# Kernel tuning notes

Hardware: AMD Instinct MI355X
Metric: run time of the kernel (lower is better)

## Reference

```python
import jax, jax.numpy as jnp
import numpy as np

EPS = 1e-5  # BatchNorm2d eps; BN in eval mode with running_mean=0, running_var=1

def conv_bn_relu(x, W, g, b):
    # x: [B, Cin, N, K]; W: [Cout, Cin] (1x1 conv). BN eval: (y-0)/sqrt(1+eps)*g + b, then ReLU.
    y = jnp.einsum('oc,bcnk->bonk', W, x)
    scale = (g / jnp.sqrt(1.0 + EPS))[None, :, None, None]
    return jax.nn.relu(y * scale + b[None, :, None, None])

def gather_neighbour(pc, idx):
    # pc: [B, N, d]; idx: [B, N, K] -> [B, N, K, d]
    B, N, K = idx.shape
    flat = idx.reshape(B, N * K, 1)
    return jnp.take_along_axis(pc, flat, axis=1).reshape(B, N, K, pc.shape[-1])

def setup_inputs() -> dict:
    B, N, K, D, H = 4, 40960, 16, 64, 32  # H = D // rfa_param
    key = jax.random.key(0)
    ks = jax.random.split(key, 16)
    inp = {
        'feature': jax.random.normal(ks[0], (B, D, N, 1), jnp.float32),
        'xyz': jax.random.normal(ks[1], (B, N, 3), jnp.float32),
        'neigh_idx': jax.random.randint(ks[2], (B, N, K), 0, N, jnp.int64),
        'W1': jax.random.normal(ks[3], (H, 10), jnp.float32) * 0.1,
        'W2': jax.random.normal(ks[4], (H, D), jnp.float32) * 0.1,
        'W3': jax.random.normal(ks[5], (H, 2 * H), jnp.float32) * 0.1,
        'W4': jax.random.normal(ks[6], (D, 2 * H), jnp.float32) * 0.1,
    }
    for i, h in zip(range(1, 5), (H, H, H, D)):
        inp[f'g{i}'] = jax.random.uniform(ks[6 + i], (h,), jnp.float32) + 0.5
        inp[f'b{i}'] = jax.random.normal(ks[10 + i], (h,), jnp.float32) * 0.1
    return inp

def reference(feature, xyz, W1, g1, b1, W2, g2, b2, W3, g3, b3, W4, g4, b4, neigh_idx):
    B, N, K = neigh_idx.shape
    # relative position encoding -> [B, N, K, 10]
    neighbor_xyz = gather_neighbour(xyz, neigh_idx)
    xyz_tile = jnp.broadcast_to(xyz[:, :, None, :], (B, N, K, 3))
    relative_xyz = xyz_tile - neighbor_xyz
    relative_dis = jnp.sqrt(jnp.sum(relative_xyz ** 2, axis=-1, keepdims=True))
    f_xyz = jnp.concatenate([relative_dis, relative_xyz, xyz_tile, neighbor_xyz], axis=-1)
    f_xyz = jnp.transpose(f_xyz, (0, 3, 1, 2))          # [B, 10, N, K]
    f_xyz = conv_bn_relu(f_xyz, W1, g1, b1)             # [B, H, N, K]
    f = conv_bn_relu(feature, W2, g2, b2)               # [B, H, N, 1]
    f_pts = jnp.transpose(f[..., 0], (0, 2, 1))         # [B, N, H]
    f_neighbours = gather_neighbour(f_pts, neigh_idx)   # [B, N, K, H]
    f_neighbours = jnp.transpose(f_neighbours, (0, 3, 1, 2))  # [B, H, N, K]
    f_concat = jnp.concatenate([f_neighbours, f_xyz], axis=1)  # [B, 2H, N, K]
    f_concat = conv_bn_relu(f_concat, W3, g3, b3)       # [B, H, N, K]
    f_concat = jnp.max(f_concat, axis=3, keepdims=True)  # max pooling over neighbors
    f = jnp.concatenate([f_concat, f], axis=1)          # [B, 2H, N, 1]
    return conv_bn_relu(f, W4, g4, b4)                  # [B, D, N, 1]
```

## Files before the change

kernel.cpp:

```cpp
#include <hip/hip_runtime.h>
#include <math.h>
#include <stdint.h>

typedef __bf16 bf16_t;
typedef bf16_t bf16x8 __attribute__((ext_vector_type(8)));
typedef bf16_t bf16x4 __attribute__((ext_vector_type(4)));
typedef float  f32x4  __attribute__((ext_vector_type(4)));

#define MFMA16(a, b, c) __builtin_amdgcn_mfma_f32_16x16x32_bf16(a, b, c, 0, 0, 0)

constexpr float BN_INV = 0.999995000037499687f;
constexpr int G2   = 2;
constexpr int RECB = 80;

__device__ __forceinline__ void agather16(const void* g, void* l) {
    __builtin_amdgcn_global_load_lds(
        (const __attribute__((address_space(1))) void*)g,
        (__attribute__((address_space(3))) void*)l, 16, 0, 0);
}

__global__ __launch_bounds__(256) void rfa_k1(
    const float* __restrict__ feature, const float* __restrict__ xyz,
    const float* __restrict__ W2, const float* __restrict__ g2, const float* __restrict__ b2,
    const float* __restrict__ W3, const float* __restrict__ g3,
    const float* __restrict__ W4, const float* __restrict__ g4,
    char* __restrict__ rec, bf16_t* __restrict__ gW3f, bf16_t* __restrict__ gW4f,
    int N, int nwaves)
{
    int tid = threadIdx.x;
    if (blockIdx.x == 0) {
        {
            int f = tid >> 6, l = tid & 63;
            int h = (f >> 1) * 16 + (l & 15), ks = f & 1, q = l >> 4;
            float sc = g3[h] * BN_INV;
            const float* src = W3 + h * 64 + ks * 32 + q * 8;
            bf16x8 v;
            #pragma unroll
            for (int j = 0; j < 8; ++j) v[j] = (bf16_t)(src[j] * sc);
            *(bf16x8*)(gW3f + ((size_t)f * 64 + l) * 8) = v;
        }
        for (int s = tid; s < 512; s += 256) {
            int f = s >> 6, l = s & 63;
            int o = (f >> 1) * 16 + (l & 15), ks = f & 1, q = l >> 4;
            float sc = g4[o] * BN_INV;
            const float* src = W4 + o * 64 + ks * 32 + q * 8;
            bf16x8 v;
            #pragma unroll
            for (int j = 0; j < 8; ++j) v[j] = (bf16_t)(src[j] * sc);
            *(bf16x8*)(gW4f + ((size_t)f * 64 + l) * 8) = v;
        }
    }

    int gtid = blockIdx.x * 256 + tid;
    int w = gtid >> 6, lane = gtid & 63;
    if (w >= nwaves) return;
    int pt = lane & 15, quad = lane >> 4;
    int T0 = w * 64;
    int b  = T0 / N;
    int n0 = T0 - b * N;

    {
        size_t p = (size_t)T0 + lane;
        float4 v = make_float4(xyz[p * 3], xyz[p * 3 + 1], xyz[p * 3 + 2], 0.f);
        *(float4*)(rec + p * RECB + 64) = v;
    }

    bf16x8 A[2][2];
    #pragma unroll
    for (int mt = 0; mt < 2; ++mt) {
        int h = mt * 16 + pt;
        float sc = g2[h] * BN_INV;
        #pragma unroll
        for (int ks = 0; ks < 2; ++ks) {
            const float* src = W2 + h * 64 + ks * 32 + quad * 8;
            bf16x8 v;
            #pragma unroll
            for (int j = 0; j < 8; ++j) v[j] = (bf16_t)(src[j] * sc);
            A[mt][ks] = v;
        }
    }
    float b2r[8];
    #pragma unroll
    for (int mt = 0; mt < 2; ++mt)
        #pragma unroll
        for (int r = 0; r < 4; ++r) b2r[mt * 4 + r] = b2[mt * 16 + quad * 4 + r];

    const float* fb = feature + (size_t)b * 64 * N;

    #pragma unroll
    for (int g = 0; g < 4; ++g) {
        int nn = n0 + g * 16 + pt;
        size_t T = (size_t)T0 + g * 16 + pt;
        bf16x8 Bf[2];
        #pragma unroll
        for (int ks = 0; ks < 2; ++ks) {
            bf16x8 v;
            #pragma unroll
            for (int j = 0; j < 8; ++j)
                v[j] = (bf16_t)fb[(size_t)(ks * 32 + quad * 8 + j) * N + nn];
            Bf[ks] = v;
        }
        f32x4 acc[2] = {f32x4{0,0,0,0}, f32x4{0,0,0,0}};
        #pragma unroll
        for (int mt = 0; mt < 2; ++mt) {
            acc[mt] = MFMA16(A[mt][0], Bf[0], acc[mt]);
            acc[mt] = MFMA16(A[mt][1], Bf[1], acc[mt]);
        }
        #pragma unroll
        for (int mt = 0; mt < 2; ++mt) {
            bf16x4 o;
            #pragma unroll
            for (int r = 0; r < 4; ++r)
                o[r] = (bf16_t)fmaxf(acc[mt][r] + b2r[mt * 4 + r], 0.f);
            *(bf16x4*)(rec + T * RECB + mt * 32 + quad * 8) = o;
        }
    }
}

__global__ __launch_bounds__(256) void rfa_k2(
    const char* __restrict__ rec, const int* __restrict__ nidx,
    const float* __restrict__ W1, const float* __restrict__ g1, const float* __restrict__ b1,
    const float* __restrict__ b3, const float* __restrict__ b4,
    const bf16_t* __restrict__ gW3f, const bf16_t* __restrict__ gW4f,
    float* __restrict__ out, int N)
{
    __shared__ __align__(16) char sAsync[4][8192];

    int tid = threadIdx.x;
    int lane = tid & 63, wv = tid >> 6;
    int n = lane & 15, quad = lane >> 4;

    int blk  = blockIdx.x;
    int b    = (blk & 7) >> 1;
    int slot = (blk >> 3) * 2 + (blk & 1);
    int grp0 = slot * (4 * G2) + wv * G2;
    int base = b * N;

    bf16x8 A3[2][2];
    #pragma unroll
    for (int mt = 0; mt < 2; ++mt)
        #pragma unroll
        for (int ks = 0; ks < 2; ++ks)
            A3[mt][ks] = *(const bf16x8*)(gW3f + ((size_t)(mt * 2 + ks) * 64 + lane) * 8);

    float a8[8], V0[8], V1[8], V2[8];
    #pragma unroll
    for (int j = 0; j < 8; ++j) {
        int c = quad * 8 + j;
        float s1 = g1[c] * BN_INV;
        const float* wp = W1 + c * 10;
        a8[j] = wp[0] * s1;
        V0[j] = (wp[7] - wp[1]) * s1;
        V1[j] = (wp[8] - wp[2]) * s1;
        V2[j] = (wp[9] - wp[3]) * s1;
    }
    float b3r[8];
    #pragma unroll
    for (int mt = 0; mt < 2; ++mt)
        #pragma unroll
        for (int r = 0; r < 4; ++r) b3r[mt * 4 + r] = b3[mt * 16 + quad * 4 + r];

    const char* rb = rec + (size_t)base * RECB;
    char* fjs = &sAsync[wv][0];
    char* pns = &sAsync[wv][4096];

    for (int gi = 0; gi < G2; ++gi) {
        int grp  = grp0 + gi;
        int nloc = grp * 16;
        size_t tg = (size_t)base + nloc + n;

        float4 ps = *(const float4*)(rec + tg * RECB + 64);
        float hoist[8];
        #pragma unroll
        for (int j = 0; j < 8; ++j) {
            int c = quad * 8 + j;
            float s1 = g1[c] * BN_INV;
            const float* wp = W1 + c * 10;
            hoist[j] = b1[c] + ((wp[1] + wp[4]) * ps.x + (wp[2] + wp[5]) * ps.y +
                                (wp[3] + wp[6]) * ps.z) * s1;
        }

        int j16[16];
        #pragma unroll
        for (int q4 = 0; q4 < 4; ++q4) {
            int4 v = *(const int4*)(nidx + tg * 16 + q4 * 4);
            j16[q4 * 4 + 0] = v.x; j16[q4 * 4 + 1] = v.y;
            j16[q4 * 4 + 2] = v.z; j16[q4 * 4 + 3] = v.w;
        }
        int jq[4];
        #pragma unroll
        for (int kb = 0; kb < 4; ++kb)
            jq[kb] = nidx[tg * 16 + kb * 4 + quad];

        asm volatile("s_waitcnt vmcnt(0)" ::: "memory");

        #pragma unroll
        for (int kb = 0; kb < 4; ++kb)
            agather16(rb + (size_t)jq[kb] * RECB + 64, pns + kb * 1024 + lane * 16);
        #pragma unroll
        for (int k0 = 0; k0 < 4; ++k0)
            agather16(rb + (size_t)j16[k0] * RECB + quad * 16, fjs + k0 * 1024 + lane * 16);

        f32x4 mx0 = {-3.0e38f, -3.0e38f, -3.0e38f, -3.0e38f};
        f32x4 mx1 = {-3.0e38f, -3.0e38f, -3.0e38f, -3.0e38f};

        #pragma unroll
        for (int k = 0; k < 16; ++k) {
            if (k <= 12)      asm volatile("s_waitcnt vmcnt(3)" ::: "memory");
            else if (k == 13) asm volatile("s_waitcnt vmcnt(2)" ::: "memory");
            else if (k == 14) asm volatile("s_waitcnt vmcnt(1)" ::: "memory");
            else              asm volatile("s_waitcnt vmcnt(0)" ::: "memory");

            bf16x8 Bj = *(const bf16x8*)(fjs + (k & 3) * 1024 + lane * 16);
            f32x4  p4 = *(const f32x4*)(pns + (k >> 2) * 1024 + ((k & 3) * 16 + n) * 16);
            asm volatile("s_waitcnt lgkmcnt(0)" ::: "memory");

            if (k + 4 < 16)
                agather16(rb + (size_t)j16[k + 4] * RECB + quad * 16,
                          fjs + (k & 3) * 1024 + lane * 16);

            float rx = ps.x - p4[0], ry = ps.y - p4[1], rz = ps.z - p4[2];
            float dist = sqrtf(rx * rx + ry * ry + rz * rz);

            bf16x8 Bx;
            #pragma unroll
            for (int c = 0; c < 8; ++c) {
                float v = fmaf(a8[c], dist, hoist[c]);
                v = fmaf(V0[c], p4[0], v);
                v = fmaf(V1[c], p4[1], v);
                v = fmaf(V2[c], p4[2], v);
                Bx[c] = (bf16_t)fmaxf(v, 0.f);
            }

            f32x4 ac0 = {0,0,0,0}, ac1 = {0,0,0,0};
            ac0 = MFMA16(A3[0][0], Bj, ac0);
            ac0 = MFMA16(A3[0][1], Bx, ac0);
            ac1 = MFMA16(A3[1][0], Bj, ac1);
            ac1 = MFMA16(A3[1][1], Bx, ac1);
            #pragma unroll
            for (int r = 0; r < 4; ++r) {
                mx0[r] = fmaxf(mx0[r], ac0[r]);
                mx1[r] = fmaxf(mx1[r], ac1[r]);
            }
        }

        float* bounce = (float*)pns;
        #pragma unroll
        for (int r = 0; r < 4; ++r) {
            bounce[(quad * 4 + r) * 18 + n]      = fmaxf(mx0[r] + b3r[r], 0.f);
            bounce[(16 + quad * 4 + r) * 18 + n] = fmaxf(mx1[r] + b3r[4 + r], 0.f);
        }
        asm volatile("s_waitcnt lgkmcnt(0)" ::: "memory");
        bf16x8 Bm;
        #pragma unroll
        for (int jj = 0; jj < 8; ++jj)
            Bm[jj] = (bf16_t)bounce[(quad * 8 + jj) * 18 + n];

        bf16x8 Bs = *(const bf16x8*)(rec + tg * RECB + quad * 16);

        #pragma unroll
        for (int mt = 0; mt < 4; ++mt) {
            bf16x8 A40 = *(const bf16x8*)(gW4f + ((size_t)(mt * 2 + 0) * 64 + lane) * 8);
            bf16x8 A41 = *(const bf16x8*)(gW4f + ((size_t)(mt * 2 + 1) * 64 + lane) * 8);
            float4 bv  = *(const float4*)(b4 + mt * 16 + quad * 4);
            f32x4 acc = {0,0,0,0};
            acc = MFMA16(A40, Bm, acc);
            acc = MFMA16(A41, Bs, acc);
            out[((size_t)b * 64 + mt * 16 + quad * 4 + 0) * N + nloc + n] = fmaxf(acc[0] + bv.x, 0.f);
            out[((size_t)b * 64 + mt * 16 + quad * 4 + 1) * N + nloc + n] = fmaxf(acc[1] + bv.y, 0.f);
            out[((size_t)b * 64 + mt * 16 + quad * 4 + 2) * N + nloc + n] = fmaxf(acc[2] + bv.z, 0.f);
            out[((size_t)b * 64 + mt * 16 + quad * 4 + 3) * N + nloc + n] = fmaxf(acc[3] + bv.w, 0.f);
        }
        asm volatile("s_waitcnt lgkmcnt(0)" ::: "memory");
    }
}

extern "C" void kernel_launch(void* const* d_in, const int* in_sizes, int n_in,
                              void* d_out, int out_size, void* d_ws, size_t ws_size,
                              hipStream_t stream) {
    const float* feature = (const float*)d_in[0];
    const float* xyz     = (const float*)d_in[1];
    const int*   nidx    = (const int*)  d_in[2];
    const float* W1      = (const float*)d_in[3];
    const float* W2      = (const float*)d_in[4];
    const float* W3      = (const float*)d_in[5];
    const float* W4      = (const float*)d_in[6];
    const float* g1 = (const float*)d_in[7];
    const float* b1 = (const float*)d_in[8];
    const float* g2 = (const float*)d_in[9];
    const float* b2 = (const float*)d_in[10];
    const float* g3 = (const float*)d_in[11];
    const float* b3 = (const float*)d_in[12];
    const float* g4 = (const float*)d_in[13];
    const float* b4 = (const float*)d_in[14];
    float* out = (float*)d_out;

    const int B = 4;
    const int N = in_sizes[1] / (B * 3);
    const int total = B * N;

    char*   rec  = (char*)d_ws;
    bf16_t* gW3f = (bf16_t*)(rec + (size_t)total * RECB);
    bf16_t* gW4f = gW3f + 4 * 64 * 8;

    const int nw1  = total / 64;
    const int blk1 = (nw1 + 3) / 4;
    const int blk2 = total / (64 * G2);

    rfa_k1<<<blk1, 256, 0, stream>>>(feature, xyz, W2, g2, b2, W3, g3, W4, g4,
                                     rec, gW3f, gW4f, N, nw1);
    rfa_k2<<<blk2, 256, 0, stream>>>(rec, nidx, W1, g1, b1, b3, b4,
                                     gW3f, gW4f, out, N);
}
```

Before: 195.3 us.

## Split point records and issue all neighbour gathers up front per wave

Replaces the interleaved 80-byte per-point record with a packed bf16 feature array and a separate float4 xyz array. Each wave now handles one 16-point group, issues all 16 neighbour-feature gathers into LDS at once, and drains them with descending vmcnt waits instead of a 4-deep ring. Blocks shrink to 128 threads with a 40KB LDS footprint. The aim is more memory-level parallelism for the random gathers, at the cost of higher LDS use per block and possibly lower occupancy.

```diff
diff --git a/kernel.cpp b/kernel.cpp
--- a/kernel.cpp
+++ b/kernel.cpp
@@ -10,8 +10,6 @@
 #define MFMA16(a, b, c) __builtin_amdgcn_mfma_f32_16x16x32_bf16(a, b, c, 0, 0, 0)
 
 constexpr float BN_INV = 0.999995000037499687f;
-constexpr int G2   = 2;
-constexpr int RECB = 80;
 
 __device__ __forceinline__ void agather16(const void* g, void* l) {
     __builtin_amdgcn_global_load_lds(
@@ -19,12 +17,15 @@
         (__attribute__((address_space(3))) void*)l, 16, 0, 0);
 }
 
+#define WAITV(n) asm volatile("s_waitcnt vmcnt(" #n ")" ::: "memory")
+
 __global__ __launch_bounds__(256) void rfa_k1(
     const float* __restrict__ feature, const float* __restrict__ xyz,
     const float* __restrict__ W2, const float* __restrict__ g2, const float* __restrict__ b2,
     const float* __restrict__ W3, const float* __restrict__ g3,
     const float* __restrict__ W4, const float* __restrict__ g4,
-    char* __restrict__ rec, bf16_t* __restrict__ gW3f, bf16_t* __restrict__ gW4f,
+    bf16_t* __restrict__ fbf, float4* __restrict__ xyz4,
+    bf16_t* __restrict__ gW3f, bf16_t* __restrict__ gW4f,
     int N, int nwaves)
 {
     int tid = threadIdx.x;
@@ -61,8 +62,7 @@
 
     {
         size_t p = (size_t)T0 + lane;
-        float4 v = make_float4(xyz[p * 3], xyz[p * 3 + 1], xyz[p * 3 + 2], 0.f);
-        *(float4*)(rec + p * RECB + 64) = v;
+        xyz4[p] = make_float4(xyz[p * 3], xyz[p * 3 + 1], xyz[p * 3 + 2], 0.f);
     }
 
     bf16x8 A[2][2];
@@ -112,19 +112,20 @@
             #pragma unroll
             for (int r = 0; r < 4; ++r)
                 o[r] = (bf16_t)fmaxf(acc[mt][r] + b2r[mt * 4 + r], 0.f);
-            *(bf16x4*)(rec + T * RECB + mt * 32 + quad * 8) = o;
+            *(bf16x4*)(fbf + T * 32 + mt * 16 + quad * 4) = o;
         }
     }
 }
 
-__global__ __launch_bounds__(256) void rfa_k2(
-    const char* __restrict__ rec, const int* __restrict__ nidx,
+__global__ __launch_bounds__(128) void rfa_k2(
+    const bf16_t* __restrict__ fbf, const float4* __restrict__ xyz4,
+    const int* __restrict__ nidx,
     const float* __restrict__ W1, const float* __restrict__ g1, const float* __restrict__ b1,
     const float* __restrict__ b3, const float* __restrict__ b4,
     const bf16_t* __restrict__ gW3f, const bf16_t* __restrict__ gW4f,
     float* __restrict__ out, int N)
 {
-    __shared__ __align__(16) char sAsync[4][8192];
+    __shared__ __align__(16) char sAsync[2][20480];
 
     int tid = threadIdx.x;
     int lane = tid & 63, wv = tid >> 6;
@@ -133,7 +134,8 @@
     int blk  = blockIdx.x;
     int b    = (blk & 7) >> 1;
     int slot = (blk >> 3) * 2 + (blk & 1);
-    int grp0 = slot * (4 * G2) + wv * G2;
+    int grp  = slot * 2 + wv;
+    int nloc = grp * 16;
     int base = b * N;
 
     bf16x8 A3[2][2];
@@ -160,118 +162,121 @@
         #pragma unroll
         for (int r = 0; r < 4; ++r) b3r[mt * 4 + r] = b3[mt * 16 + quad * 4 + r];
 
-    const char* rb = rec + (size_t)base * RECB;
+    const bf16_t* fb  = fbf  + (size_t)base * 32;
+    const float4* xzb = xyz4 + (size_t)base;
     char* fjs = &sAsync[wv][0];
-    char* pns = &sAsync[wv][4096];
-
-    for (int gi = 0; gi < G2; ++gi) {
-        int grp  = grp0 + gi;
-        int nloc = grp * 16;
-        size_t tg = (size_t)base + nloc + n;
-
-        float4 ps = *(const float4*)(rec + tg * RECB + 64);
-        float hoist[8];
-        #pragma unroll
-        for (int j = 0; j < 8; ++j) {
-            int c = quad * 8 + j;
-            float s1 = g1[c] * BN_INV;
-            const float* wp = W1 + c * 10;
-            hoist[j] = b1[c] + ((wp[1] + wp[4]) * ps.x + (wp[2] + wp[5]) * ps.y +
-                                (wp[3] + wp[6]) * ps.z) * s1;
-        }
-
-        int j16[16];
-        #pragma unroll
-        for (int q4 = 0; q4 < 4; ++q4) {
-            int4 v = *(const int4*)(nidx + tg * 16 + q4 * 4);
-            j16[q4 * 4 + 0] = v.x; j16[q4 * 4 + 1] = v.y;
-            j16[q4 * 4 + 2] = v.z; j16[q4 * 4 + 3] = v.w;
-        }
-        int jq[4];
-        #pragma unroll
-        for (int kb = 0; kb < 4; ++kb)
-            jq[kb] = nidx[tg * 16 + kb * 4 + quad];
-
-        asm volatile("s_waitcnt vmcnt(0)" ::: "memory");
-
-        #pragma unroll
-        for (int kb = 0; kb < 4; ++kb)
-            agather16(rb + (size_t)jq[kb] * RECB + 64, pns + kb * 1024 + lane * 16);
-        #pragma unroll
-        for (int k0 = 0; k0 < 4; ++k0)
-            agather16(rb + (size_t)j16[k0] * RECB + quad * 16, fjs + k0 * 1024 + lane * 16);
-
-        f32x4 mx0 = {-3.0e38f, -3.0e38f, -3.0e38f, -3.0e38f};
-        f32x4 mx1 = {-3.0e38f, -3.0e38f, -3.0e38f, -3.0e38f};
-
-        #pragma unroll
-        for (int k = 0; k < 16; ++k) {
-            if (k <= 12)      asm volatile("s_waitcnt vmcnt(3)" ::: "memory");
-            else if (k == 13) asm volatile("s_waitcnt vmcnt(2)" ::: "memory");
-            else if (k == 14) asm volatile("s_waitcnt vmcnt(1)" ::: "memory");
-            else              asm volatile("s_waitcnt vmcnt(0)" ::: "memory");
-
-            bf16x8 Bj = *(const bf16x8*)(fjs + (k & 3) * 1024 + lane * 16);
-            f32x4  p4 = *(const f32x4*)(pns + (k >> 2) * 1024 + ((k & 3) * 16 + n) * 16);
-            asm volatile("s_waitcnt lgkmcnt(0)" ::: "memory");
-
-            if (k + 4 < 16)
-                agather16(rb + (size_t)j16[k + 4] * RECB + quad * 16,
-                          fjs + (k & 3) * 1024 + lane * 16);
-
-            float rx = ps.x - p4[0], ry = ps.y - p4[1], rz = ps.z - p4[2];
-            float dist = sqrtf(rx * rx + ry * ry + rz * rz);
-
-            bf16x8 Bx;
-            #pragma unroll
-            for (int c = 0; c < 8; ++c) {
-                float v = fmaf(a8[c], dist, hoist[c]);
-                v = fmaf(V0[c], p4[0], v);
-                v = fmaf(V1[c], p4[1], v);
-                v = fmaf(V2[c], p4[2], v);
-                Bx[c] = (bf16_t)fmaxf(v, 0.f);
-            }
-
-            f32x4 ac0 = {0,0,0,0}, ac1 = {0,0,0,0};
-            ac0 = MFMA16(A3[0][0], Bj, ac0);
-            ac0 = MFMA16(A3[0][1], Bx, ac0);
-            ac1 = MFMA16(A3[1][0], Bj, ac1);
-            ac1 = MFMA16(A3[1][1], Bx, ac1);
-            #pragma unroll
-            for (int r = 0; r < 4; ++r) {
-                mx0[r] = fmaxf(mx0[r], ac0[r]);
-                mx1[r] = fmaxf(mx1[r], ac1[r]);
-            }
-        }
-
-        float* bounce = (float*)pns;
+    char* pns = &sAsync[wv][16384];
+
+    size_t tg = (size_t)base + nloc + n;
+
+    float4 ps = xyz4[tg];
+    float hoist[8];
+    #pragma unroll
+    for (int j = 0; j < 8; ++j) {
+        int c = quad * 8 + j;
+        float s1 = g1[c] * BN_INV;
+        const float* wp = W1 + c * 10;
+        hoist[j] = b1[c] + ((wp[1] + wp[4]) * ps.x + (wp[2] + wp[5]) * ps.y +
+                            (wp[3] + wp[6]) * ps.z) * s1;
+    }
+
+    int j16[16];
+    #pragma unroll
+    for (int q4 = 0; q4 < 4; ++q4) {
+        int4 v = *(const int4*)(nidx + tg * 16 + q4 * 4);
+        j16[q4 * 4 + 0] = v.x; j16[q4 * 4 + 1] = v.y;
+        j16[q4 * 4 + 2] = v.z; j16[q4 * 4 + 3] = v.w;
+    }
+    int jq[4];
+    #pragma unroll
+    for (int kb = 0; kb < 4; ++kb)
+        jq[kb] = nidx[tg * 16 + kb * 4 + quad];
+
+    asm volatile("s_waitcnt vmcnt(0)" ::: "memory");
+
+    #pragma unroll
+    for (int kb = 0; kb < 4; ++kb)
+        agather16(xzb + jq[kb], pns + kb * 1024 + lane * 16);
+    #pragma unroll
+    for (int k = 0; k < 16; ++k)
+        agather16(fb + (size_t)j16[k] * 32 + quad * 8, fjs + k * 1024 + lane * 16);
+
+    f32x4 mx0 = {-3.0e38f, -3.0e38f, -3.0e38f, -3.0e38f};
+    f32x4 mx1 = {-3.0e38f, -3.0e38f, -3.0e38f, -3.0e38f};
+
+    #pragma unroll
+    for (int k = 0; k < 16; ++k) {
+        if      (k == 0)  WAITV(15);
+        else if (k == 1)  WAITV(14);
+        else if (k == 2)  WAITV(13);
+        else if (k == 3)  WAITV(12);
+        else if (k == 4)  WAITV(11);
+        else if (k == 5)  WAITV(10);
+        else if (k == 6)  WAITV(9);
+        else if (k == 7)  WAITV(8);
+        else if (k == 8)  WAITV(7);
+        else if (k == 9)  WAITV(6);
+        else if (k == 10) WAITV(5);
+        else if (k == 11) WAITV(4);
+        else if (k == 12) WAITV(3);
+        else if (k == 13) WAITV(2);
+        else if (k == 14) WAITV(1);
+        else              WAITV(0);
+
+        bf16x8 Bj = *(const bf16x8*)(fjs + k * 1024 + lane * 16);
+        f32x4  p4 = *(const f32x4*)(pns + (k >> 2) * 1024 + ((k & 3) * 16 + n) * 16);
+
+        float rx = ps.x - p4[0], ry = ps.y - p4[1], rz = ps.z - p4[2];
+        float dist = sqrtf(rx * rx + ry * ry + rz * rz);
+
+        bf16x8 Bx;
+        #pragma unroll
+        for (int c = 0; c < 8; ++c) {
+            float v = fmaf(a8[c], dist, hoist[c]);
+            v = fmaf(V0[c], p4[0], v);
+            v = fmaf(V1[c], p4[1], v);
+            v = fmaf(V2[c], p4[2], v);
+            Bx[c] = (bf16_t)fmaxf(v, 0.f);
+        }
+
+        f32x4 ac0 = {0,0,0,0}, ac1 = {0,0,0,0};
+        ac0 = MFMA16(A3[0][0], Bj, ac0);
+        ac0 = MFMA16(A3[0][1], Bx, ac0);
+        ac1 = MFMA16(A3[1][0], Bj, ac1);
+        ac1 = MFMA16(A3[1][1], Bx, ac1);
         #pragma unroll
         for (int r = 0; r < 4; ++r) {
-            bounce[(quad * 4 + r) * 18 + n]      = fmaxf(mx0[r] + b3r[r], 0.f);
-            bounce[(16 + quad * 4 + r) * 18 + n] = fmaxf(mx1[r] + b3r[4 + r], 0.f);
-        }
-        asm volatile("s_waitcnt lgkmcnt(0)" ::: "memory");
-        bf16x8 Bm;
-        #pragma unroll
-        for (int jj = 0; jj < 8; ++jj)
-            Bm[jj] = (bf16_t)bounce[(quad * 8 + jj) * 18 + n];
-
-        bf16x8 Bs = *(const bf16x8*)(rec + tg * RECB + quad * 16);
-
-        #pragma unroll
-        for (int mt = 0; mt < 4; ++mt) {
-            bf16x8 A40 = *(const bf16x8*)(gW4f + ((size_t)(mt * 2 + 0) * 64 + lane) * 8);
-            bf16x8 A41 = *(const bf16x8*)(gW4f + ((size_t)(mt * 2 + 1) * 64 + lane) * 8);
-            float4 bv  = *(const float4*)(b4 + mt * 16 + quad * 4);
-            f32x4 acc = {0,0,0,0};
-            acc = MFMA16(A40, Bm, acc);
-            acc = MFMA16(A41, Bs, acc);
-            out[((size_t)b * 64 + mt * 16 + quad * 4 + 0) * N + nloc + n] = fmaxf(acc[0] + bv.x, 0.f);
-            out[((size_t)b * 64 + mt * 16 + quad * 4 + 1) * N + nloc + n] = fmaxf(acc[1] + bv.y, 0.f);
-            out[((size_t)b * 64 + mt * 16 + quad * 4 + 2) * N + nloc + n] = fmaxf(acc[2] + bv.z, 0.f);
-            out[((size_t)b * 64 + mt * 16 + quad * 4 + 3) * N + nloc + n] = fmaxf(acc[3] + bv.w, 0.f);
-        }
-        asm volatile("s_waitcnt lgkmcnt(0)" ::: "memory");
+            mx0[r] = fmaxf(mx0[r], ac0[r]);
+            mx1[r] = fmaxf(mx1[r], ac1[r]);
+        }
+    }
+
+    float* bounce = (float*)fjs;
+    #pragma unroll
+    for (int r = 0; r < 4; ++r) {
+        bounce[(quad * 4 + r) * 18 + n]      = fmaxf(mx0[r] + b3r[r], 0.f);
+        bounce[(16 + quad * 4 + r) * 18 + n] = fmaxf(mx1[r] + b3r[4 + r], 0.f);
+    }
+    asm volatile("s_waitcnt lgkmcnt(0)" ::: "memory");
+    bf16x8 Bm;
+    #pragma unroll
+    for (int jj = 0; jj < 8; ++jj)
+        Bm[jj] = (bf16_t)bounce[(quad * 8 + jj) * 18 + n];
+
+    bf16x8 Bs = *(const bf16x8*)(fb + (size_t)(nloc + n) * 32 + quad * 8);
+
+    #pragma unroll
+    for (int mt = 0; mt < 4; ++mt) {
+        bf16x8 A40 = *(const bf16x8*)(gW4f + ((size_t)(mt * 2 + 0) * 64 + lane) * 8);
+        bf16x8 A41 = *(const bf16x8*)(gW4f + ((size_t)(mt * 2 + 1) * 64 + lane) * 8);
+        float4 bv  = *(const float4*)(b4 + mt * 16 + quad * 4);
+        f32x4 acc = {0,0,0,0};
+        acc = MFMA16(A40, Bm, acc);
+        acc = MFMA16(A41, Bs, acc);
+        out[((size_t)b * 64 + mt * 16 + quad * 4 + 0) * N + nloc + n] = fmaxf(acc[0] + bv.x, 0.f);
+        out[((size_t)b * 64 + mt * 16 + quad * 4 + 1) * N + nloc + n] = fmaxf(acc[1] + bv.y, 0.f);
+        out[((size_t)b * 64 + mt * 16 + quad * 4 + 2) * N + nloc + n] = fmaxf(acc[2] + bv.z, 0.f);
+        out[((size_t)b * 64 + mt * 16 + quad * 4 + 3) * N + nloc + n] = fmaxf(acc[3] + bv.w, 0.f);
     }
 }
 
@@ -299,16 +304,17 @@
     const int N = in_sizes[1] / (B * 3);
     const int total = B * N;
 
-    char*   rec  = (char*)d_ws;
-    bf16_t* gW3f = (bf16_t*)(rec + (size_t)total * RECB);
+    bf16_t* fbf  = (bf16_t*)d_ws;
+    float4* xyz4 = (float4*)((char*)d_ws + (size_t)total * 64);
+    bf16_t* gW3f = (bf16_t*)((char*)xyz4 + (size_t)total * 16);
     bf16_t* gW4f = gW3f + 4 * 64 * 8;
 
     const int nw1  = total / 64;
     const int blk1 = (nw1 + 3) / 4;
-    const int blk2 = total / (64 * G2);
+    const int blk2 = total / 32;
 
     rfa_k1<<<blk1, 256, 0, stream>>>(feature, xyz, W2, g2, b2, W3, g3, W4, g4,
-                                     rec, gW3f, gW4f, N, nw1);
-    rfa_k2<<<blk2, 256, 0, stream>>>(rec, nidx, W1, g1, b1, b3, b4,
+                                     fbf, xyz4, gW3f, gW4f, N, nw1);
+    rfa_k2<<<blk2, 128, 0, stream>>>(fbf, xyz4, nidx, W1, g1, b1, b3, b4,
                                      gW3f, gW4f, out, N);
 }
```

New measurement: 215.4 us. +10.3%, slower.
